# Optimization experiments

Measured on AMD Instinct MI355X. Metric: run time of the kernel, lower is better.

Reference implementation:

```python
import jax, jax.numpy as jnp
import numpy as np


def setup_inputs() -> dict:
    key = jax.random.key(0)
    k1, k2, k3, k4 = jax.random.split(key, 4)
    d_in, d_out = 1024, 1024
    x = jax.random.normal(k1, (4, 2048, d_in), dtype=jnp.float32)
    # nn.Linear weights, stored as [d_in, d_out] for x @ W (torch stores transpose)
    s = 1.0 / np.sqrt(d_in)
    Wq = jax.random.normal(k2, (d_in, d_out), dtype=jnp.float32) * s
    Wk = jax.random.normal(k3, (d_in, d_out), dtype=jnp.float32) * s
    Wv = jax.random.normal(k4, (d_in, d_out), dtype=jnp.float32) * s
    return {"x": x, "Wq": Wq, "Wk": Wk, "Wv": Wv}


def reference(x, Wq, Wk, Wv):
    # x: [b, s, d_in]; projections (no bias)
    q = jnp.einsum('bsi,io->bso', x, Wq)
    k = jnp.einsum('bsi,io->bso', x, Wk)
    v = jnp.einsum('bsi,io->bso', x, Wv)
    d_out = k.shape[-1]
    scores = jnp.einsum('bqd,bkd->bqk', q, k) / jnp.sqrt(jnp.float32(d_out))
    seq_len = x.shape[1]
    causal = jnp.tril(jnp.ones((seq_len, seq_len), dtype=bool))  # [s, s]
    scores = jnp.where(causal[None, :, :], scores, -jnp.inf)
    weights = jax.nn.softmax(scores, axis=-1)
    return jnp.einsum('bqk,bkd->bqd', weights, v)
```

## Files before the change

### kernel.cpp

```cpp
#include <hip/hip_runtime.h>

typedef __attribute__((ext_vector_type(8))) short bf16x8;
typedef __attribute__((ext_vector_type(4))) float f32x4;
typedef unsigned int u32;

__device__ __forceinline__ unsigned short f2bf(float f) {
  union { float f; unsigned int u; } a; a.f = f;
  unsigned int u = a.u;
  u += 0x7FFFu + ((u >> 16) & 1u);
  return (unsigned short)(u >> 16);
}

__device__ __forceinline__ void gload16(const unsigned short* g, unsigned short* l) {
  __builtin_amdgcn_global_load_lds((const __attribute__((address_space(1))) u32*)g,
                                   (__attribute__((address_space(3))) u32*)l, 16, 0, 0);
}

#define BK 64

template<int MODE>
__global__ __launch_bounds__(256, 4)
void gemm_bt(const unsigned short* __restrict__ A,
             const unsigned short* __restrict__ Bm,
             float* __restrict__ Cf,
             float* __restrict__ Cf2,
             unsigned short* __restrict__ Cb,
             int K, long aBatch, long bBatch, long cBatch, float scale)
{
  constexpr int NI    = 2;
  constexpr int BROWS = 16;
  constexpr int BG    = 2;

  int z, bm0 = 0, bn, p = 0;
  if (MODE == 2) {
    int flat = blockIdx.x + 272 * blockIdx.z;
    int rm   = (flat & 7) * 136 + (flat >> 3);
    z = rm / 272;
    int f = rm % 272;
    int r = (int)((sqrtf((float)(4 * f + 1)) - 1.0f) * 0.5f);
    while ((r + 1) * (r + 2) <= f) r++;
    while (r * (r + 1) > f) r--;
    bm0 = r * 128;
    bn  = (f - r * (r + 1)) * 64;
  } else if (MODE == 3) {
    int flat = blockIdx.x + 16 * blockIdx.y + 128 * blockIdx.z;
    int rm   = (flat & 7) * 64 + (flat >> 3);
    z  = rm >> 7;
    p  = (rm >> 4) & 7;
    bn = (rm & 15) * 64;
  } else {
    z   = blockIdx.z;
    bm0 = blockIdx.y * 128;
    bn  = blockIdx.x * 64;
  }

  A  += (long)z * aBatch;
  Bm += (long)z * bBatch;
  if (MODE == 2) { Cb += (long)z * cBatch; Cf += (long)z * 2048; }
  if (MODE == 3) { Cf += (long)z * cBatch; Cf2 += (long)z * 2048; }

  __shared__ __align__(16) unsigned short As[128 * BK];
  __shared__ __align__(16) unsigned short Bs[64 * BK];

  int tid  = threadIdx.x;
  int wave = tid >> 6, lane = tid & 63;
  int wm = wave * 32, wn = 0;
  int quad = lane >> 4, l16 = lane & 15;

  int r8 = lane >> 3;
  int c  = (lane & 7) ^ r8;
  const unsigned short* Bg = Bm + (long)(bn + wave * BROWS + r8) * K + c * 8;
  unsigned short* Al = &As[(wave * 32) * BK];
  unsigned short* Bl = &Bs[(wave * BROWS) * BK];

  const int nseg = (MODE == 3) ? 2 : 1;
  for (int seg = 0; seg < nseg; seg++) {
    int bm   = (MODE == 3) ? ((seg == 0) ? (15 - p) * 128 : p * 128) : bm0;
    int Keff = (MODE == 3) ? ((seg == 0) ? 128 * (16 - p) : 128 * (p + 1)) : K;
    const unsigned short* Ag = A + (long)(bm + wave * 32 + r8) * K + c * 8;

    f32x4 acc[NI][4] = {};

    for (int k0 = 0; k0 < Keff; k0 += BK) {
#pragma unroll
      for (int g = 0; g < 4; g++)
        gload16(Ag + k0 + (long)g * 8 * K, Al + g * 8 * BK);
#pragma unroll
      for (int g = 0; g < BG; g++)
        gload16(Bg + k0 + (long)g * 8 * K, Bl + g * 8 * BK);
      __syncthreads();

#pragma unroll
      for (int h = 0; h < 2; h++) {
        bf16x8 af[NI], bfr[4];
#pragma unroll
        for (int i = 0; i < NI; i++)
          af[i]  = *(const bf16x8*)&As[(wm + i * 16 + l16) * BK + (((quad + 4 * h) ^ (l16 & 7)) * 8)];
#pragma unroll
        for (int j = 0; j < 4; j++)
          bfr[j] = *(const bf16x8*)&Bs[(wn + j * 16 + l16) * BK + (((quad + 4 * h) ^ (l16 & 7)) * 8)];
#pragma unroll
        for (int i = 0; i < NI; i++)
#pragma unroll
          for (int j = 0; j < 4; j++)
            acc[i][j] = __builtin_amdgcn_mfma_f32_16x16x32_bf16(af[i], bfr[j], acc[i][j], 0, 0, 0);
      }
      __syncthreads();
    }

#pragma unroll
    for (int i = 0; i < NI; i++) {
      int grow0 = bm + wm + i * 16 + quad * 4;
      if (MODE == 2) {
#pragma unroll
        for (int r = 0; r < 4; r++) {
          int grow = grow0 + r;
          float rowpart = 0.f;
#pragma unroll
          for (int j = 0; j < 4; j++) {
            int gcol = bn + j * 16 + l16;
            float e = (gcol <= grow) ? __expf(acc[i][j][r] * scale) : 0.f;
            rowpart += e;
            Cb[(long)grow * 2048 + gcol] = f2bf(e);
          }
          rowpart += __shfl_xor(rowpart, 1);
          rowpart += __shfl_xor(rowpart, 2);
          rowpart += __shfl_xor(rowpart, 4);
          rowpart += __shfl_xor(rowpart, 8);
          if (l16 == 0) atomicAdd(&Cf[grow], rowpart);
        }
      } else if (MODE == 3) {
        float rinv[4];
#pragma unroll
        for (int r = 0; r < 4; r++) rinv[r] = 1.0f / Cf2[grow0 + r];
#pragma unroll
        for (int j = 0; j < 4; j++) {
          int gcol = bn + j * 16 + l16;
#pragma unroll
          for (int r = 0; r < 4; r++)
            Cf[(long)(grow0 + r) * 1024 + gcol] = acc[i][j][r] * rinv[r];
        }
      } else {
#pragma unroll
        for (int j = 0; j < 4; j++) {
          int gcol = bn + j * 16 + l16;
#pragma unroll
          for (int r = 0; r < 4; r++)
            Cb[(long)(grow0 + r) * 1024 + gcol] = f2bf(acc[i][j][r]);
        }
      }
    }
  }
}

__global__ __launch_bounds__(512, 2)
void gemm_tv8(const unsigned short* __restrict__ A,
              const unsigned short* __restrict__ Bm,
              unsigned short* __restrict__ Cb)
{
  constexpr int NT = 16;
  constexpr int SLOT = 256 * 64;
  __shared__ __align__(16) unsigned short AsL[2 * SLOT];
  __shared__ __align__(16) unsigned short BsL[2 * SLOT];

  const int tid  = threadIdx.x;
  const int wave = tid >> 6, lane = tid & 63;
  const int quad = lane >> 4, l16 = lane & 15;
  const int wr = wave >> 2, wc = wave & 3;
  const int flat = blockIdx.x + 8 * blockIdx.y;
  const int rm   = (flat & 7) * 32 + (flat >> 3);
  const int bm = (rm >> 3) * 256;
  const int bn = (rm & 7) * 256;

  const int l8 = lane >> 3;
  const int sc = ((lane & 7) ^ l8) * 8;
  const unsigned short* Ag = A  + (long)(bm + wave * 8 + l8) * 1024 + sc;
  const unsigned short* Bg = Bm + (long)(bn + (wave >> 2) * 64 + (wave & 3) * 8 + l8) * 1024 + sc;

#define STGA(base, h, t) {                                                      \
    gload16(Ag + (long)((h) * 64) * 1024 + (t) * 64,        (base) + ((h) * 128 + wave * 8) * 64);      \
    gload16(Ag + (long)(128 + (h) * 64) * 1024 + (t) * 64,  (base) + ((h) * 128 + 64 + wave * 8) * 64); }
#define STGB(base, h, t) {                                                      \
    gload16(Bg + (long)((h) * 32) * 1024 + (t) * 64,        (base) + ((h) * 128 + wave * 8) * 64);      \
    gload16(Bg + (long)(128 + (h) * 32) * 1024 + (t) * 64,  (base) + ((h) * 128 + 64 + wave * 8) * 64); }

#define RD_A(afX, src, qm) _Pragma("unroll") for (int i = 0; i < 4; ++i)        \
    _Pragma("unroll") for (int h2 = 0; h2 < 2; ++h2)                            \
      afX[i][h2] = *(const bf16x8*)&(src)[((qm) * 128 + wr * 64 + i * 16 + l16) * 64 + (((quad + 4 * h2) ^ (l16 & 7)) * 8)];
#define RD_B(bfX, src, qn) _Pragma("unroll") for (int j = 0; j < 2; ++j)        \
    _Pragma("unroll") for (int h2 = 0; h2 < 2; ++h2)                            \
      bfX[j][h2] = *(const bf16x8*)&(src)[((qn) * 128 + wc * 32 + j * 16 + l16) * 64 + (((quad + 4 * h2) ^ (l16 & 7)) * 8)];
#define MFMA16(afX, bfX, MI0, NJ0) {                                            \
    __builtin_amdgcn_s_setprio(1);                                              \
    _Pragma("unroll") for (int i = 0; i < 4; ++i)                               \
      _Pragma("unroll") for (int j = 0; j < 2; ++j)                             \
        _Pragma("unroll") for (int h2 = 0; h2 < 2; ++h2)                        \
          acc[(MI0) + i][(NJ0) + j] =                                           \
            __builtin_amdgcn_mfma_f32_16x16x32_bf16(afX[i][h2], bfX[j][h2], acc[(MI0) + i][(NJ0) + j], 0, 0, 0); \
    __builtin_amdgcn_s_setprio(0); }

  f32x4 acc[8][4] = {};

  STGA(AsL, 0, 0) STGB(BsL, 0, 0)
  STGA(AsL, 1, 0) STGB(BsL, 1, 0)
  STGB(BsL + SLOT, 0, 1) STGA(AsL + SLOT, 1, 1)
  asm volatile("s_waitcnt vmcnt(4)" ::: "memory");
  __builtin_amdgcn_sched_barrier(0);
  __builtin_amdgcn_s_barrier();

#pragma unroll 1
  for (int u = 0; u < NT; ++u) {
    const int b = u & 1;
    const unsigned short* Asb = AsL + b * SLOT;
    const unsigned short* Bsb = BsL + b * SLOT;
    unsigned short* Asn = AsL + (b ^ 1) * SLOT;
    unsigned short* Bsn = BsL + (b ^ 1) * SLOT;
    unsigned short* Asc = AsL + b * SLOT;
    unsigned short* Bsc = BsL + b * SLOT;

    bf16x8 af0[4][2], af1[4][2], bf0[2][2], bf1[2][2];

    RD_A(af0, Asb, 0)
    RD_B(bf0, Bsb, 0)
    if (u + 1 < NT) { STGA(Asn, 0, u + 1) STGB(Bsn, 1, u + 1) }
    __builtin_amdgcn_s_barrier();
    MFMA16(af0, bf0, 0, 0)
    __builtin_amdgcn_s_barrier();

    RD_A(af1, Asb, 1)
    if (u + 2 < NT) STGB(Bsc, 0, u + 2)
    __builtin_amdgcn_s_barrier();
    MFMA16(af1, bf0, 4, 0)
    __builtin_amdgcn_s_barrier();

    RD_B(bf1, Bsb, 1)
    if (u + 2 < NT) STGA(Asc, 1, u + 2)
    __builtin_amdgcn_s_barrier();
    MFMA16(af1, bf1, 4, 2)
    __builtin_amdgcn_s_barrier();

    if (u < NT - 2)       { asm volatile("s_waitcnt vmcnt(4)" ::: "memory"); }
    else if (u == NT - 2) { asm volatile("s_waitcnt vmcnt(0)" ::: "memory"); }
    __builtin_amdgcn_sched_barrier(0);
    __builtin_amdgcn_s_barrier();
    MFMA16(af0, bf1, 0, 2)
    __builtin_amdgcn_s_barrier();
  }
#undef STGA
#undef STGB
#undef RD_A
#undef RD_B
#undef MFMA16

#pragma unroll
  for (int mi = 0; mi < 8; ++mi) {
    int grow0 = bm + wr * 128 + mi * 16 + quad * 4;
#pragma unroll
    for (int nj = 0; nj < 4; ++nj) {
      int gcol = bn + wc * 64 + nj * 16 + l16;
      int which = gcol >> 10;
      int col = gcol & 1023;
      if (which == 0) {
#pragma unroll
        for (int r = 0; r < 4; r++)
          Cb[(long)(grow0 + r) * 1024 + col] = f2bf(acc[mi][nj][r]);
      } else {
        unsigned short* Vt = Cb + (long)8192 * 1024;
        int bb = grow0 >> 11, s = grow0 & 2047;
        ushort4 pk;
        pk.x = f2bf(acc[mi][nj][0]); pk.y = f2bf(acc[mi][nj][1]);
        pk.z = f2bf(acc[mi][nj][2]); pk.w = f2bf(acc[mi][nj][3]);
        *(ushort4*)(Vt + ((long)bb * 1024 + col) * 2048 + s) = pk;
      }
    }
  }
}

__global__ __launch_bounds__(256)
void prep(const float* __restrict__ x,
          const float* __restrict__ W0, const float* __restrict__ W1,
          const float* __restrict__ W2,
          unsigned short* __restrict__ Xb,
          unsigned short* __restrict__ Wqb, unsigned short* __restrict__ Wkb,
          unsigned short* __restrict__ WvT,
          float* __restrict__ rsum)
{
  __shared__ float tile[32][33];
  int b = blockIdx.x;
  if (b < 8192) {
    long i = ((long)b * 256 + threadIdx.x) * 4;
    float4 v = *(const float4*)(x + i);
    ushort4 o;
    o.x = f2bf(v.x); o.y = f2bf(v.y); o.z = f2bf(v.z); o.w = f2bf(v.w);
    *(ushort4*)(Xb + i) = o;
  } else if (b < 10240) {
    int t = b - 8192;
    const float* W    = (t < 1024) ? W0 : W1;
    unsigned short* D = (t < 1024) ? Wqb : Wkb;
    long i = ((long)(t & 1023) * 256 + threadIdx.x) * 4;
    float4 v = *(const float4*)(W + i);
    ushort4 o;
    o.x = f2bf(v.x); o.y = f2bf(v.y); o.z = f2bf(v.z); o.w = f2bf(v.w);
    *(ushort4*)(D + i) = o;
  } else if (b < 11264) {
    int q = b - 10240;
    int kb = (q >> 5) * 32, nb = (q & 31) * 32;
    int tx = threadIdx.x & 31, ty = threadIdx.x >> 5;
    for (int r = ty; r < 32; r += 8)
      tile[r][tx] = W2[(long)(kb + r) * 1024 + nb + tx];
    __syncthreads();
    for (int r = ty; r < 32; r += 8)
      WvT[(long)(nb + r) * 1024 + kb + tx] = f2bf(tile[tx][r]);
  } else {
    long i = ((long)(b - 11264) * 256 + threadIdx.x) * 4;
    float4 zz = {0.f, 0.f, 0.f, 0.f};
    *(float4*)(rsum + i) = zz;
  }
}

extern "C" void kernel_launch(void* const* d_in, const int* in_sizes, int n_in,
                              void* d_out, int out_size, void* d_ws, size_t ws_size,
                              hipStream_t stream) {
  const float* x  = (const float*)d_in[0];
  const float* Wq = (const float*)d_in[1];
  const float* Wk = (const float*)d_in[2];
  const float* Wv = (const float*)d_in[3];
  float* out = (float*)d_out;

  unsigned short* Xb  = (unsigned short*)d_ws;
  unsigned short* Wqb = Xb  + (long)8192 * 1024;
  unsigned short* Wkb = Wqb + (long)1024 * 1024;
  unsigned short* TVB = Wkb + (long)1024 * 1024;
  unsigned short* T   = TVB + (long)2048 * 1024;
  unsigned short* Vt  = T   + (long)8192 * 1024;
  unsigned short* E   = Vt  + (long)8192 * 1024;
  float* rsum         = (float*)(E + (long)4 * 2048 * 2048);

  prep<<<11272, 256, 0, stream>>>(x, Wq, Wk, Wv, Xb, Wqb, Wkb,
                                  TVB + (long)1024 * 1024, rsum);

  gemm_bt<1><<<dim3(16, 8, 1), 256, 0, stream>>>(Wkb, Wqb, nullptr, nullptr, TVB,
      1024, 0, 0, 0, 1.f);

  gemm_tv8<<<dim3(8, 32, 1), 512, 0, stream>>>(Xb, TVB, T);

  gemm_bt<2><<<dim3(272, 1, 4), 256, 0, stream>>>(T, Xb, rsum, nullptr, E, 1024,
      (long)2048 * 1024, (long)2048 * 1024, (long)2048 * 2048, 0.03125f);

  gemm_bt<3><<<dim3(16, 8, 4), 256, 0, stream>>>(E, Vt, out, rsum, nullptr, 2048,
      (long)2048 * 2048, (long)1024 * 2048, (long)2048 * 1024, 1.f);
}
```

Before: 204.4 us.

## Split scores and weight-product GEMMs into dedicated kernels with retuned tiles

The causal scores GEMM moves into its own kernel, which uses 2 waves per 128x64 tile, each wave computing 64x64 (4x4 MFMA tiles). That raises register-level reuse and halves the threads per block. The Wk·Wq^T product gets a separate 64x64-tile kernel, launched on 256 blocks instead of 128, to fill more CUs. The trade-off is fewer waves per block in the scores kernel, which may reduce latency hiding, and more accumulator registers per thread.

```diff
diff --git a/kernel.cpp b/kernel.cpp
--- a/kernel.cpp
+++ b/kernel.cpp
@@ -32,17 +32,7 @@
   constexpr int BG    = 2;
 
   int z, bm0 = 0, bn, p = 0;
-  if (MODE == 2) {
-    int flat = blockIdx.x + 272 * blockIdx.z;
-    int rm   = (flat & 7) * 136 + (flat >> 3);
-    z = rm / 272;
-    int f = rm % 272;
-    int r = (int)((sqrtf((float)(4 * f + 1)) - 1.0f) * 0.5f);
-    while ((r + 1) * (r + 2) <= f) r++;
-    while (r * (r + 1) > f) r--;
-    bm0 = r * 128;
-    bn  = (f - r * (r + 1)) * 64;
-  } else if (MODE == 3) {
+  if (MODE == 3) {
     int flat = blockIdx.x + 16 * blockIdx.y + 128 * blockIdx.z;
     int rm   = (flat & 7) * 64 + (flat >> 3);
     z  = rm >> 7;
@@ -56,7 +46,6 @@
 
   A  += (long)z * aBatch;
   Bm += (long)z * bBatch;
-  if (MODE == 2) { Cb += (long)z * cBatch; Cf += (long)z * 2048; }
   if (MODE == 3) { Cf += (long)z * cBatch; Cf2 += (long)z * 2048; }
 
   __shared__ __align__(16) unsigned short As[128 * BK];
@@ -64,7 +53,7 @@
 
   int tid  = threadIdx.x;
   int wave = tid >> 6, lane = tid & 63;
-  int wm = wave * 32, wn = 0;
+  int wm = wave * 32;
   int quad = lane >> 4, l16 = lane & 15;
 
   int r8 = lane >> 3;
@@ -98,7 +87,7 @@
           af[i]  = *(const bf16x8*)&As[(wm + i * 16 + l16) * BK + (((quad + 4 * h) ^ (l16 & 7)) * 8)];
 #pragma unroll
         for (int j = 0; j < 4; j++)
-          bfr[j] = *(const bf16x8*)&Bs[(wn + j * 16 + l16) * BK + (((quad + 4 * h) ^ (l16 & 7)) * 8)];
+          bfr[j] = *(const bf16x8*)&Bs[(j * 16 + l16) * BK + (((quad + 4 * h) ^ (l16 & 7)) * 8)];
 #pragma unroll
         for (int i = 0; i < NI; i++)
 #pragma unroll
@@ -111,25 +100,7 @@
 #pragma unroll
     for (int i = 0; i < NI; i++) {
       int grow0 = bm + wm + i * 16 + quad * 4;
-      if (MODE == 2) {
-#pragma unroll
-        for (int r = 0; r < 4; r++) {
-          int grow = grow0 + r;
-          float rowpart = 0.f;
-#pragma unroll
-          for (int j = 0; j < 4; j++) {
-            int gcol = bn + j * 16 + l16;
-            float e = (gcol <= grow) ? __expf(acc[i][j][r] * scale) : 0.f;
-            rowpart += e;
-            Cb[(long)grow * 2048 + gcol] = f2bf(e);
-          }
-          rowpart += __shfl_xor(rowpart, 1);
-          rowpart += __shfl_xor(rowpart, 2);
-          rowpart += __shfl_xor(rowpart, 4);
-          rowpart += __shfl_xor(rowpart, 8);
-          if (l16 == 0) atomicAdd(&Cf[grow], rowpart);
-        }
-      } else if (MODE == 3) {
+      if (MODE == 3) {
         float rinv[4];
 #pragma unroll
         for (int r = 0; r < 4; r++) rinv[r] = 1.0f / Cf2[grow0 + r];
@@ -149,6 +120,149 @@
             Cb[(long)(grow0 + r) * 1024 + gcol] = f2bf(acc[i][j][r]);
         }
       }
+    }
+  }
+}
+
+__global__ __launch_bounds__(256, 4)
+void mt64(const unsigned short* __restrict__ Wkb,
+          const unsigned short* __restrict__ Wqb,
+          unsigned short* __restrict__ Mt)
+{
+  int bm = blockIdx.y * 64, bn = blockIdx.x * 64;
+  __shared__ __align__(16) unsigned short As[64 * 64];
+  __shared__ __align__(16) unsigned short Bs[64 * 64];
+
+  int tid  = threadIdx.x;
+  int wave = tid >> 6, lane = tid & 63;
+  int quad = lane >> 4, l16 = lane & 15;
+  int r8 = lane >> 3;
+  int c  = (lane & 7) ^ r8;
+  const unsigned short* Ag = Wkb + (long)(bm + wave * 16 + r8) * 1024 + c * 8;
+  const unsigned short* Bg = Wqb + (long)(bn + wave * 16 + r8) * 1024 + c * 8;
+  unsigned short* Al = &As[(wave * 16) * 64];
+  unsigned short* Bl = &Bs[(wave * 16) * 64];
+
+  f32x4 acc[4] = {};
+
+  for (int k0 = 0; k0 < 1024; k0 += 64) {
+#pragma unroll
+    for (int g = 0; g < 2; g++)
+      gload16(Ag + k0 + (long)g * 8 * 1024, Al + g * 8 * 64);
+#pragma unroll
+    for (int g = 0; g < 2; g++)
+      gload16(Bg + k0 + (long)g * 8 * 1024, Bl + g * 8 * 64);
+    __syncthreads();
+
+#pragma unroll
+    for (int h = 0; h < 2; h++) {
+      bf16x8 af, bfr[4];
+      af = *(const bf16x8*)&As[(wave * 16 + l16) * 64 + (((quad + 4 * h) ^ (l16 & 7)) * 8)];
+#pragma unroll
+      for (int j = 0; j < 4; j++)
+        bfr[j] = *(const bf16x8*)&Bs[(j * 16 + l16) * 64 + (((quad + 4 * h) ^ (l16 & 7)) * 8)];
+#pragma unroll
+      for (int j = 0; j < 4; j++)
+        acc[j] = __builtin_amdgcn_mfma_f32_16x16x32_bf16(af, bfr[j], acc[j], 0, 0, 0);
+    }
+    __syncthreads();
+  }
+
+  int grow0 = bm + wave * 16 + quad * 4;
+#pragma unroll
+  for (int j = 0; j < 4; j++) {
+    int gcol = bn + j * 16 + l16;
+#pragma unroll
+    for (int r = 0; r < 4; r++)
+      Mt[(long)(grow0 + r) * 1024 + gcol] = f2bf(acc[j][r]);
+  }
+}
+
+__global__ __launch_bounds__(128, 3)
+void scores2wz(const unsigned short* __restrict__ T,
+               const unsigned short* __restrict__ Xb,
+               float* __restrict__ rsum,
+               unsigned short* __restrict__ E,
+               float scale)
+{
+  int flat = blockIdx.x + 272 * blockIdx.z;
+  int rm   = (flat & 7) * 136 + (flat >> 3);
+  int z = rm / 272;
+  int f = rm % 272;
+  int r = (int)((sqrtf((float)(4 * f + 1)) - 1.0f) * 0.5f);
+  while ((r + 1) * (r + 2) <= f) r++;
+  while (r * (r + 1) > f) r--;
+  int bm0 = r * 128;
+  int bn  = (f - r * (r + 1)) * 64;
+
+  const unsigned short* A = T  + (long)z * 2048 * 1024;
+  const unsigned short* B = Xb + (long)z * 2048 * 1024;
+  unsigned short* Cb = E + (long)z * 2048 * 2048;
+  float* Cf = rsum + (long)z * 2048;
+
+  __shared__ __align__(16) unsigned short As[128 * BK];
+  __shared__ __align__(16) unsigned short Bs[64 * BK];
+
+  int tid  = threadIdx.x;
+  int wave = tid >> 6, lane = tid & 63;
+  int quad = lane >> 4, l16 = lane & 15;
+  int wm   = wave * 64;
+
+  int r8 = lane >> 3;
+  int c  = (lane & 7) ^ r8;
+  const unsigned short* Ag = A + (long)(bm0 + wave * 64 + r8) * 1024 + c * 8;
+  const unsigned short* Bg = B + (long)(bn  + wave * 32 + r8) * 1024 + c * 8;
+  unsigned short* Al = &As[(wave * 64) * BK];
+  unsigned short* Bl = &Bs[(wave * 32) * BK];
+
+  f32x4 acc[4][4] = {};
+
+  for (int k0 = 0; k0 < 1024; k0 += BK) {
+#pragma unroll
+    for (int g = 0; g < 8; g++)
+      gload16(Ag + k0 + (long)g * 8 * 1024, Al + g * 8 * BK);
+#pragma unroll
+    for (int g = 0; g < 4; g++)
+      gload16(Bg + k0 + (long)g * 8 * 1024, Bl + g * 8 * BK);
+    __syncthreads();
+
+#pragma unroll
+    for (int h = 0; h < 2; h++) {
+      bf16x8 af[4], bfr[4];
+#pragma unroll
+      for (int i = 0; i < 4; i++)
+        af[i]  = *(const bf16x8*)&As[(wm + i * 16 + l16) * BK + (((quad + 4 * h) ^ (l16 & 7)) * 8)];
+#pragma unroll
+      for (int j = 0; j < 4; j++)
+        bfr[j] = *(const bf16x8*)&Bs[(j * 16 + l16) * BK + (((quad + 4 * h) ^ (l16 & 7)) * 8)];
+#pragma unroll
+      for (int i = 0; i < 4; i++)
+#pragma unroll
+        for (int j = 0; j < 4; j++)
+          acc[i][j] = __builtin_amdgcn_mfma_f32_16x16x32_bf16(af[i], bfr[j], acc[i][j], 0, 0, 0);
+    }
+    __syncthreads();
+  }
+
+#pragma unroll
+  for (int i = 0; i < 4; i++) {
+    int grow0 = bm0 + wm + i * 16 + quad * 4;
+#pragma unroll
+    for (int rr = 0; rr < 4; rr++) {
+      int grow = grow0 + rr;
+      float rowpart = 0.f;
+#pragma unroll
+      for (int j = 0; j < 4; j++) {
+        int gcol = bn + j * 16 + l16;
+        float e = (gcol <= grow) ? __expf(acc[i][j][rr] * scale) : 0.f;
+        rowpart += e;
+        Cb[(long)grow * 2048 + gcol] = f2bf(e);
+      }
+      rowpart += __shfl_xor(rowpart, 1);
+      rowpart += __shfl_xor(rowpart, 2);
+      rowpart += __shfl_xor(rowpart, 4);
+      rowpart += __shfl_xor(rowpart, 8);
+      if (l16 == 0) atomicAdd(&Cf[grow], rowpart);
     }
   }
 }
@@ -339,13 +453,11 @@
   prep<<<11272, 256, 0, stream>>>(x, Wq, Wk, Wv, Xb, Wqb, Wkb,
                                   TVB + (long)1024 * 1024, rsum);
 
-  gemm_bt<1><<<dim3(16, 8, 1), 256, 0, stream>>>(Wkb, Wqb, nullptr, nullptr, TVB,
-      1024, 0, 0, 0, 1.f);
+  mt64<<<dim3(16, 16, 1), 256, 0, stream>>>(Wkb, Wqb, TVB);
 
   gemm_tv8<<<dim3(8, 32, 1), 512, 0, stream>>>(Xb, TVB, T);
 
-  gemm_bt<2><<<dim3(272, 1, 4), 256, 0, stream>>>(T, Xb, rsum, nullptr, E, 1024,
-      (long)2048 * 1024, (long)2048 * 1024, (long)2048 * 2048, 0.03125f);
+  scores2wz<<<dim3(272, 1, 4), 128, 0, stream>>>(T, Xb, rsum, E, 0.03125f);
 
   gemm_bt<3><<<dim3(16, 8, 4), 256, 0, stream>>>(E, Vt, out, rsum, nullptr, 2048,
       (long)2048 * 2048, (long)1024 * 2048, (long)2048 * 1024, 1.f);
```

New measurement: 201.9 us, median of 3. No clear change (-1.2%).
